# Performance work log

Hardware: AMD Instinct MI355X
Metric: run time of the kernel (lower is better)

## Reference

```python
import jax, jax.numpy as jnp
import numpy as np
import math

B, L, D = 8, 2048, 768
ORDER, EMB = 128, 5
FFT = 2 * L
MIN_DECAY = math.log(0.01) / 1.5   # slow_decay_pct = 1.5
MAX_DECAY = math.log(0.01) / 0.3   # fast_decay_pct = 0.3
SHIFT = 0.0


def _pos_emb(seq_len, emb_dim):
    # pos_emb_init from the source: [t, Re(z), Im(z)] with bands = (emb_dim-1)//2
    bands = (emb_dim - 1) // 2
    t = jnp.linspace(0.0, 1.0, seq_len)[None, :, None]
    t_res = jnp.linspace(0.0, seq_len - 1, seq_len)[None, :, None]
    w = 2.0 * jnp.pi * t_res / seq_len
    f = jnp.linspace(1e-4, bands - 1, bands)[None, None]
    zc = jnp.exp(-1j * f * w)
    return jnp.concatenate([t, zc.real, zc.imag], axis=-1).astype(jnp.float32)  # (1, L, EMB)


def setup_inputs() -> dict:
    key = jax.random.key(0)
    ks = jax.random.split(key, 16)
    s = 0.02
    return {
        "u": jax.random.normal(ks[0], (B, L, D), jnp.float32),
        "in_W": jax.random.normal(ks[1], (D, 3 * D), jnp.float32) * s,
        "in_b": jnp.zeros((3 * D,), jnp.float32),
        "out_W": jax.random.normal(ks[2], (D, D), jnp.float32) * s,
        "out_b": jnp.zeros((D,), jnp.float32),
        "x1_s": jax.random.normal(ks[3], (D, 4), jnp.float32) * 0.25,
        "x2_s": jax.random.normal(ks[4], (D, 4), jnp.float32) * 0.25,
        "v_s": jax.random.normal(ks[5], (D, 4), jnp.float32) * 0.25,
        "x1_sb": jax.random.normal(ks[6], (D,), jnp.float32) * 0.1,
        "x2_sb": jax.random.normal(ks[7], (D,), jnp.float32) * 0.1,
        "v_sb": jax.random.normal(ks[8], (D,), jnp.float32) * 0.1,
        "D_bias": jax.random.normal(ks[9], (D,), jnp.float32),
        "z": _pos_emb(L, EMB),
        "sin_freq": 10.0 * jnp.ones((1, ORDER), jnp.float32),   # hyena_w = 10
        "eo_mat": jax.random.normal(ks[10], (1, EMB, ORDER), jnp.float32) * 0.3,
        "eo_bias": jnp.zeros((1, ORDER), jnp.float32),
        "oo1_mat": jax.random.normal(ks[11], (1, ORDER, ORDER), jnp.float32) * 0.08,
        "oo1_bias": jnp.zeros((1, ORDER), jnp.float32),
        "oo2_mat": jax.random.normal(ks[12], (1, ORDER, ORDER), jnp.float32) * 0.08,
        "oo2_bias": jnp.zeros((1, ORDER), jnp.float32),
        "oh_mat": jax.random.normal(ks[13], (1, ORDER, D), jnp.float32) * 0.08,
    }


def _depthwise4(x, w, b):
    # torch Conv1d(groups=3D, kernel=4, padding=3) truncated to [:L] == causal conv, left pad 3
    out = jax.lax.conv_general_dilated(
        x, w[:, None, :], window_strides=(1,), padding=[(3, 0)],
        dimension_numbers=("NCH", "OIH", "NCH"), feature_group_count=x.shape[1])
    return out + b[None, :, None]


def _hyena_filter(z, sin_freq, eo_mat, eo_bias, oo1_mat, oo1_bias, oo2_mat, oo2_bias, oh_mat):
    # then exponential decay modulation (exp_mod_in_place_fwd), channels=1, reverse=0.
    f = sin_freq[:, None, :]                                       # (1, 1, ORDER)
    h = jnp.sin(f * (jnp.einsum("cle,ceo->clo", z, eo_mat) + eo_bias[:, None, :]))
    h = jnp.sin(f * (jnp.einsum("clo,cop->clp", h, oo1_mat) + oo1_bias[:, None, :]))
    h = jnp.sin(f * (jnp.einsum("clo,cop->clp", h, oo2_mat) + oo2_bias[:, None, :]))
    k = jnp.einsum("clo,coh->clh", h, oh_mat)                      # (1, L, D)
    t = jnp.linspace(0.0, 1.0, k.shape[1])
    deltas = jnp.abs(jnp.linspace(MIN_DECAY, MAX_DECAY, k.shape[2]))
    k = k * (jnp.exp(-t[None, :, None] * deltas[None, None, :]) + SHIFT)
    return k[0].T                                                  # (D, L)


def _forward(u, in_W, in_b, out_W, out_b, x1_s, x2_s, v_s, x1_sb, x2_sb, v_sb,
             D_bias, z, sin_freq, eo_mat, eo_bias, oo1_mat, oo1_bias,
             oo2_mat, oo2_bias, oh_mat):
    seqlen = u.shape[1]
    k = _hyena_filter(z, sin_freq, eo_mat, eo_bias, oo1_mat, oo1_bias, oo2_mat, oo2_bias, oh_mat)
    x1x2v = u @ in_W + in_b                                        # (B, L, 3D)
    x1, x2, v = jnp.split(x1x2v, 3, axis=-1)
    x1 = jnp.transpose(x1, (0, 2, 1))                              # (B, D, L)
    x2 = jnp.transpose(x2, (0, 2, 1))
    v = jnp.transpose(v, (0, 2, 1))
    x1 = _depthwise4(x1, x1_s, x1_sb)
    x2 = _depthwise4(x2, x2_s, x2_sb)
    v = _depthwise4(v, v_s, v_sb)
    v = v * x1                                                     # first gate
    k_f = jnp.fft.rfft(k.astype(jnp.float32), n=FFT)               # (D, FFT//2+1)
    v_f = jnp.fft.rfft(v.astype(jnp.float32), n=FFT)               # (B, D, FFT//2+1)
    y = jnp.fft.irfft(v_f * k_f[None], n=FFT)[..., :seqlen]        # long FFT conv
    y = y + v * D_bias[None, :, None]                              # skip term
    y = y * x2                                                     # second gate
    y = jnp.transpose(y, (0, 2, 1))                                # (B, L, D)
    return y @ out_W + out_b


def reference(u, in_W, in_b, out_W, out_b, x1_s, x2_s, v_s, x1_sb, x2_sb, v_sb,
              D_bias, z, sin_freq, eo_mat, eo_bias, oo1_mat, oo1_bias,
              oo2_mat, oo2_bias, oh_mat):
    return _forward(u, in_W, in_b, out_W, out_b, x1_s, x2_s, v_s, x1_sb, x2_sb, v_sb,
                    D_bias, z, sin_freq, eo_mat, eo_bias, oo1_mat, oo1_bias,
                    oo2_mat, oo2_bias, oh_mat)
```

## Files before the change

### kernel.cpp

```cpp
#include <hip/hip_runtime.h>


typedef __bf16 bf16x8 __attribute__((ext_vector_type(8)));
typedef float  f32x4  __attribute__((ext_vector_type(4)));

#define AS1 __attribute__((address_space(1)))
#define AS3 __attribute__((address_space(3)))
#define GLD16(gp, lp) __builtin_amdgcn_global_load_lds((AS1 void*)(void*)(gp), (AS3 void*)(void*)(lp), 16, 0, 0)

#define PIPE_VM_BARRIER(N)  __asm__ __volatile__("s_waitcnt vmcnt(" #N ")\n\ts_barrier" ::: "memory")
#define PIPE_LGKM_BARRIER   __asm__ __volatile__("s_waitcnt lgkmcnt(0)\n\ts_barrier" ::: "memory")

__device__ __forceinline__ unsigned short f2b(float f) {
    unsigned u = __builtin_bit_cast(unsigned, f);
    unsigned r = (u + 0x7fffu + ((u >> 16) & 1u)) >> 16;
    return (unsigned short)r;
}
__device__ __forceinline__ float b2f(unsigned short h) {
    unsigned u = ((unsigned)h) << 16;
    return __builtin_bit_cast(float, u);
}
__device__ __forceinline__ float b2f_lo(unsigned u) {
    return __builtin_bit_cast(float, u << 16);
}
__device__ __forceinline__ float b2f_hi(unsigned u) {
    return __builtin_bit_cast(float, u & 0xffff0000u);
}

__device__ __forceinline__ float2 cmul(float2 a, float2 b) {
    return make_float2(a.x * b.x - a.y * b.y, a.x * b.y + a.y * b.x);
}
__device__ __forceinline__ float2 cadd(float2 a, float2 b) { return make_float2(a.x + b.x, a.y + b.y); }
__device__ __forceinline__ float2 csub(float2 a, float2 b) { return make_float2(a.x - b.x, a.y - b.y); }

#define BFLY(i,j)   { float2 ta=x[i], tb=x[j]; x[i]=cadd(ta,tb); x[j]=csub(ta,tb); }
#define BFLYW(i,j,w){ float2 ta=x[i], tb=x[j]; x[i]=cadd(ta,tb); x[j]=cmul(csub(ta,tb),(w)); }
#define BFLYI(i,j)  { float2 ta=x[i], tb=x[j]; x[i]=cadd(ta,tb); float2 tt=csub(ta,tb); x[j]=make_float2(-dd*tt.y, dd*tt.x); }
#define CSWAP(i,j)  { float2 tt=x[i]; x[i]=x[j]; x[j]=tt; }

template<int DIR, bool UZ>
__device__ __forceinline__ void dft16(float2* x) {
    const float dd = (float)DIR;
    const float C1 = 0.92387953251128674f, S1 = 0.38268343236508977f, R2 = 0.70710678118654752f;
    const float2 W1 = make_float2( C1, dd*S1);
    const float2 W2 = make_float2( R2, dd*R2);
    const float2 W3 = make_float2( S1, dd*C1);
    const float2 W5 = make_float2(-S1, dd*C1);
    const float2 W6 = make_float2(-R2, dd*R2);
    const float2 W7 = make_float2(-C1, dd*S1);
    if (UZ) {
        x[8]  = x[0];
        x[9]  = cmul(x[1], W1);
        x[10] = cmul(x[2], W2);
        x[11] = cmul(x[3], W3);
        x[12] = make_float2(-dd*x[4].y, dd*x[4].x);
        x[13] = cmul(x[5], W5);
        x[14] = cmul(x[6], W6);
        x[15] = cmul(x[7], W7);
    } else {
        BFLY(0,8); BFLYW(1,9,W1); BFLYW(2,10,W2); BFLYW(3,11,W3);
        BFLYI(4,12); BFLYW(5,13,W5); BFLYW(6,14,W6); BFLYW(7,15,W7);
    }
    BFLY(0,4);  BFLYW(1,5,W2);  BFLYI(2,6);   BFLYW(3,7,W6);
    BFLY(8,12); BFLYW(9,13,W2); BFLYI(10,14); BFLYW(11,15,W6);
    BFLY(0,2);  BFLYI(1,3);  BFLY(4,6);   BFLYI(5,7);
    BFLY(8,10); BFLYI(9,11); BFLY(12,14); BFLYI(13,15);
    BFLY(0,1); BFLY(2,3); BFLY(4,5); BFLY(6,7);
    BFLY(8,9); BFLY(10,11); BFLY(12,13); BFLY(14,15);
    CSWAP(1,8); CSWAP(2,4); CSWAP(3,12); CSWAP(5,10); CSWAP(7,14); CSWAP(11,13);
}

__device__ __forceinline__ void twiddle_mul(float2* x, float ang) {
    float s, c; __sincosf(ang, &s, &c);
    float2 w[16];
    w[1] = make_float2(c, s);
    w[2] = cmul(w[1], w[1]);
    w[3] = cmul(w[2], w[1]);  w[4] = cmul(w[2], w[2]);
    w[5] = cmul(w[4], w[1]);  w[6] = cmul(w[4], w[2]);
    w[7] = cmul(w[4], w[3]);  w[8] = cmul(w[4], w[4]);
    w[9]  = cmul(w[8], w[1]); w[10] = cmul(w[8], w[2]);
    w[11] = cmul(w[8], w[3]); w[12] = cmul(w[8], w[4]);
    w[13] = cmul(w[8], w[5]); w[14] = cmul(w[8], w[6]);
    w[15] = cmul(w[8], w[7]);
    #pragma unroll
    for (int k = 1; k < 16; ++k) x[k] = cmul(x[k], w[k]);
}

#define TWO_PI 6.283185307179586f
__device__ __forceinline__ void fft4096_fwd(float2* x, float2* lds, int t) {
    dft16<-1, true>(x);
    twiddle_mul(x, -(float)t * (TWO_PI / 4096.0f));
    #pragma unroll
    for (int k1 = 0; k1 < 16; ++k1) lds[k1 * 272 + t] = x[k1];
    __syncthreads();
    const int hi = t >> 4, lo = t & 15;
    #pragma unroll
    for (int t1 = 0; t1 < 16; ++t1) x[t1] = lds[hi * 272 + t1 * 16 + lo];
    dft16<-1, false>(x);
    twiddle_mul(x, -(float)lo * (TWO_PI / 256.0f));
    __syncthreads();
    #pragma unroll
    for (int k2 = 0; k2 < 16; ++k2) lds[t * 17 + k2] = x[k2];
    __syncthreads();
    #pragma unroll
    for (int t0 = 0; t0 < 16; ++t0) x[t0] = lds[(hi * 16 + t0) * 17 + lo];
    dft16<-1, false>(x);
}

__device__ __forceinline__ void fft4096_inv(float2* x, float2* lds, int t) {
    const int hi = t >> 4, lo = t & 15;
    dft16<1, false>(x);
    __syncthreads();
    #pragma unroll
    for (int t0 = 0; t0 < 16; ++t0) lds[(hi * 16 + t0) * 17 + lo] = x[t0];
    __syncthreads();
    #pragma unroll
    for (int k2 = 0; k2 < 16; ++k2) x[k2] = lds[t * 17 + k2];
    twiddle_mul(x, (float)lo * (TWO_PI / 256.0f));
    dft16<1, false>(x);
    __syncthreads();
    #pragma unroll
    for (int t1 = 0; t1 < 16; ++t1) lds[hi * 272 + t1 * 16 + lo] = x[t1];
    __syncthreads();
    #pragma unroll
    for (int k1 = 0; k1 < 16; ++k1) x[k1] = lds[k1 * 272 + t];
    twiddle_mul(x, (float)t * (TWO_PI / 4096.0f));
    dft16<1, false>(x);
}

__global__ __launch_bounds__(256) void filter_k_kernel(
    const float* __restrict__ z, const float* __restrict__ sf,
    const float* __restrict__ eo, const float* __restrict__ eo_b,
    const float* __restrict__ oo1, const float* __restrict__ oo1_b,
    const float* __restrict__ oo2, const float* __restrict__ oo2_b,
    const float* __restrict__ oh, float* __restrict__ kfil)
{
    __shared__ float h3buf[8][128];
    __shared__ float htmp[2][128];
    const int t = threadIdx.x;
    const int l0 = blockIdx.x * 8;
    const int half = t >> 7;
    const int o = t & 127;
    const float sfo = sf[o];
    for (int p = 0; p < 4; ++p) {
        const int li = p * 2 + half;
        const int l = l0 + li;
        float a = eo_b[o];
        #pragma unroll
        for (int e = 0; e < 5; ++e) a += z[l * 5 + e] * eo[e * 128 + o];
        htmp[half][o] = sinf(sfo * a);
        __syncthreads();
        float a2 = oo1_b[o];
        for (int q = 0; q < 128; ++q) a2 += htmp[half][q] * oo1[q * 128 + o];
        const float h2 = sinf(sfo * a2);
        __syncthreads();
        htmp[half][o] = h2;
        __syncthreads();
        float a3 = oo2_b[o];
        for (int q = 0; q < 128; ++q) a3 += htmp[half][q] * oo2[q * 128 + o];
        h3buf[li][o] = sinf(sfo * a3);
        __syncthreads();
    }
    const float MIND = -3.070113457325394f;
    const float MAXD = -15.350567286626972f;
    for (int c = 0; c < 3; ++c) {
        const int h = t + c * 256;
        float acc[8];
        #pragma unroll
        for (int li = 0; li < 8; ++li) acc[li] = 0.f;
        for (int q = 0; q < 128; ++q) {
            const float w = oh[q * 768 + h];
            #pragma unroll
            for (int li = 0; li < 8; ++li) acc[li] += h3buf[li][q] * w;
        }
        const float delta = fabsf(MIND + (MAXD - MIND) * (float)h * (1.0f / 767.0f));
        #pragma unroll
        for (int li = 0; li < 8; ++li) {
            const int l = l0 + li;
            const float tt = (float)l * (1.0f / 2047.0f);
            kfil[h * 2048 + l] = acc[li] * expf(-tt * delta);
        }
    }
}

__global__ __launch_bounds__(256, 4) void filter_fft_kernel(
    const float* __restrict__ kfil, float2* __restrict__ Kf)
{
    __shared__ float2 lds[4352];
    const int d = blockIdx.x, t = threadIdx.x;
    float2 x[16];
    #pragma unroll
    for (int r = 0; r < 8; ++r) x[r] = make_float2(kfil[d * 2048 + r * 256 + t], 0.f);
    fft4096_fwd(x, lds, t);
    #pragma unroll
    for (int k3 = 0; k3 < 16; ++k3) Kf[d * 4096 + k3 * 256 + t] = x[k3];
}

__global__ __launch_bounds__(256) void convert_u_kernel(
    const float* __restrict__ u, unsigned short* __restrict__ ub)
{
    const int g = blockIdx.x * 256 + threadIdx.x;
    const float4 v = ((const float4*)u)[g];
    uint2 o;
    o.x = (unsigned)f2b(v.x) | ((unsigned)f2b(v.y) << 16);
    o.y = (unsigned)f2b(v.z) | ((unsigned)f2b(v.w) << 16);
    ((uint2*)ub)[g] = o;
}

__global__ __launch_bounds__(256) void transpose_W_kernel(
    const float* __restrict__ W, unsigned short* __restrict__ Wt, int K, int N)
{
    __shared__ float tile[32][33];
    const int n0 = blockIdx.x * 32, k0 = blockIdx.y * 32;
    const int tx = threadIdx.x & 31, ty = threadIdx.x >> 5;
    #pragma unroll
    for (int r = 0; r < 4; ++r) {
        const int kk = ty + r * 8;
        tile[kk][tx] = W[(k0 + kk) * N + n0 + tx];
    }
    __syncthreads();
    #pragma unroll
    for (int r = 0; r < 4; ++r) {
        const int nn = ty + r * 8;
        Wt[(n0 + nn) * K + k0 + tx] = f2b(tile[tx][nn]);
    }
}

__global__ __launch_bounds__(256) void transpose_Y_kernel(
    const unsigned short* __restrict__ Y, unsigned short* __restrict__ Yt)
{
    __shared__ unsigned short tile[32][34];
    const int bx = blockIdx.x;
    const int l0 = (bx & 63) * 32;
    const int tmp = bx >> 6;
    const int d0 = (tmp % 24) * 32;
    const int b  = tmp / 24;
    const int tx = threadIdx.x & 31, ty = threadIdx.x >> 5;
    #pragma unroll
    for (int r = 0; r < 4; ++r) {
        const int dd = ty + r * 8;
        tile[dd][tx] = Y[(b * 768 + d0 + dd) * 2048 + l0 + tx];
    }
    __syncthreads();
    #pragma unroll
    for (int r = 0; r < 4; ++r) {
        const int ll = ty + r * 8;
        Yt[(b * 2048 + l0 + ll) * 768 + d0 + tx] = tile[tx][ll];
    }
}

__global__ __launch_bounds__(256, 3) void gemm_kernel(
    const unsigned short* __restrict__ A,
    const unsigned short* __restrict__ Bm,
    const float* __restrict__ bias,
    unsigned short* __restrict__ outb,
    float* __restrict__ outf,
    int mode)
{
    __shared__ __align__(16) unsigned short As[3 * 4096];
    __shared__ __align__(16) unsigned short Bs[3 * 4096];
    const int t = threadIdx.x;
    const int wv = t >> 6, lane = t & 63;
    const int row0 = (mode == 0 ? blockIdx.y : blockIdx.x) * 128;
    const int col0 = (mode == 0 ? blockIdx.x : blockIdx.y) * 128;
    const int wr = wv >> 1, wc = wv & 1;

    f32x4 acc[4][4] = {};

    const int r0 = t >> 2;
    const int r1 = r0 + 64;
    const int c0 = (t & 3) ^ (((r0 >> 1) ^ (r0 >> 3)) & 3);
    const int c1 = (t & 3) ^ (((r1 >> 1) ^ (r1 >> 3)) & 3);
    const unsigned short* gA0 = A + (row0 + r0) * 768 + c0 * 8;
    const unsigned short* gA1 = A + (row0 + r1) * 768 + c1 * 8;
    const unsigned short* gB0 = Bm + (col0 + r0) * 768 + c0 * 8;
    const unsigned short* gB1 = Bm + (col0 + r1) * 768 + c1 * 8;

    const int frow = lane & 15, kc = lane >> 4;
    int offA[4], offB[4];
    #pragma unroll
    for (int i = 0; i < 4; ++i) {
        const int ra = wr * 64 + i * 16 + frow;
        const int rb = wc * 64 + i * 16 + frow;
        offA[i] = ra * 32 + ((kc ^ (((ra >> 1) ^ (ra >> 3)) & 3)) << 3);
        offB[i] = rb * 32 + ((kc ^ (((rb >> 1) ^ (rb >> 3)) & 3)) << 3);
    }

    GLD16(gA0, (char*)As + wv * 1024);
    GLD16(gA1, (char*)As + 4096 + wv * 1024);
    GLD16(gB0, (char*)Bs + wv * 1024);
    GLD16(gB1, (char*)Bs + 4096 + wv * 1024);
    gA0 += 32; gA1 += 32; gB0 += 32; gB1 += 32;
    GLD16(gA0, (char*)As + 8192 + wv * 1024);
    GLD16(gA1, (char*)As + 8192 + 4096 + wv * 1024);
    GLD16(gB0, (char*)Bs + 8192 + wv * 1024);
    GLD16(gB1, (char*)Bs + 8192 + 4096 + wv * 1024);
    gA0 += 32; gA1 += 32; gB0 += 32; gB1 += 32;

#define GEMM_FRAG_MFMA(CUR)                                                   \
        const unsigned short* Ast = As + (CUR) * 4096;                        \
        const unsigned short* Bst = Bs + (CUR) * 4096;                        \
        bf16x8 af[4], bfr[4];                                                 \
        _Pragma("unroll") for (int i = 0; i < 4; ++i) {                       \
            af[i]  = *(const bf16x8*)(Ast + offA[i]);                         \
            bfr[i] = *(const bf16x8*)(Bst + offB[i]);                         \
        }                                                                     \
        _Pragma("unroll") for (int i = 0; i < 4; ++i)                         \
            _Pragma("unroll") for (int j = 0; j < 4; ++j)                     \
                acc[i][j] = __builtin_amdgcn_mfma_f32_16x16x32_bf16(          \
                    af[i], bfr[j], acc[i][j], 0, 0, 0);

#define GEMM_BODY(CUR, PF)                                                    \
    {                                                                         \
        GLD16(gA0, (char*)As + (PF) * 8192 + wv * 1024);                      \
        GLD16(gA1, (char*)As + (PF) * 8192 + 4096 + wv * 1024);               \
        GLD16(gB0, (char*)Bs + (PF) * 8192 + wv * 1024);                      \
        GLD16(gB1, (char*)Bs + (PF) * 8192 + 4096 + wv * 1024);               \
        gA0 += 32; gA1 += 32; gB0 += 32; gB1 += 32;                           \
        PIPE_VM_BARRIER(8);     \
        GEMM_FRAG_MFMA(CUR)                                                   \
        PIPE_LGKM_BARRIER;     \
    }

#define GEMM_TAIL(CUR, N)                                                     \
    {                                                                         \
        PIPE_VM_BARRIER(N);                                                   \
        GEMM_FRAG_MFMA(CUR)                                                   \
    }

    for (int kq = 0; kq < 7; ++kq) {
        GEMM_BODY(0, 2)
        GEMM_BODY(1, 0)
        GEMM_BODY(2, 1)
    }
    GEMM_BODY(0, 2)
    GEMM_TAIL(1, 4)
    GEMM_TAIL(2, 0)
#undef GEMM_BODY
#undef GEMM_TAIL
#undef GEMM_FRAG_MFMA

    if (mode == 0) {
        const int part = row0 / 768;
        const int bb = col0 / 2048;
        unsigned short* Xp = outb + (part * 8 + bb) * 768 * 2048;
        const int dbase = row0 - part * 768 + wr * 64 + (lane >> 4) * 4;
        const int lbase = col0 - bb * 2048 + wc * 64 + frow;
        #pragma unroll
        for (int i = 0; i < 4; ++i) {
            #pragma unroll
            for (int rr = 0; rr < 4; ++rr) {
                const int dd = dbase + i * 16 + rr;
                const float bn = bias[row0 + wr * 64 + (lane >> 4) * 4 + i * 16 + rr];
                #pragma unroll
                for (int j = 0; j < 4; ++j) {
                    const int ll = lbase + j * 16;
                    Xp[dd * 2048 + ll] = f2b(acc[i][j][rr] + bn);
                }
            }
        }
    } else {
        #pragma unroll
        for (int i = 0; i < 4; ++i) {
            #pragma unroll
            for (int rr = 0; rr < 4; ++rr) {
                const int m = row0 + wr * 64 + (lane >> 4) * 4 + i * 16 + rr;
                #pragma unroll
                for (int j = 0; j < 4; ++j) {
                    const int n = col0 + wc * 64 + j * 16 + frow;
                    outf[m * 768 + n] = acc[i][j][rr] + bias[n];
                }
            }
        }
    }
}

__device__ __forceinline__ void conv6(const unsigned short* __restrict__ p,
                                      const float* w, float bias, int t, float* out8)
{
    const uint4 m = *(const uint4*)(p + 8 * t);
    uint2 q = make_uint2(0u, 0u);
    if (t) q = *(const uint2*)(p + 8 * t - 4);
    float s[12];
    s[0] = b2f_lo(q.x); s[1] = b2f_hi(q.x); s[2] = b2f_lo(q.y); s[3] = b2f_hi(q.y);
    s[4] = b2f_lo(m.x); s[5] = b2f_hi(m.x); s[6] = b2f_lo(m.y); s[7] = b2f_hi(m.y);
    s[8] = b2f_lo(m.z); s[9] = b2f_hi(m.z); s[10] = b2f_lo(m.w); s[11] = b2f_hi(m.w);
    #pragma unroll
    for (int i = 0; i < 8; ++i)
        out8[i] = bias + w[0] * s[i + 1] + w[1] * s[i + 2] + w[2] * s[i + 3] + w[3] * s[i + 4];
}

__global__ __launch_bounds__(256, 4) void fft_conv_kernel(
    const unsigned short* __restrict__ X, const float2* __restrict__ Kf,
    const float* __restrict__ x1_s, const float* __restrict__ x2_s, const float* __restrict__ v_s,
    const float* __restrict__ x1_sb, const float* __restrict__ x2_sb, const float* __restrict__ v_sb,
    const float* __restrict__ D_bias, unsigned short* __restrict__ Y)
{
    __shared__ __align__(16) float2 lds[4352];
    unsigned* ldsu = (unsigned*)lds;
    const int d = blockIdx.x, jp = blockIdx.y, t = threadIdx.x;
    const int b0 = jp * 2, b1 = b0 + 1;

    float w1[4], w2[4], wv[4];
    #pragma unroll
    for (int j = 0; j < 4; ++j) { w1[j] = x1_s[d * 4 + j]; w2[j] = x2_s[d * 4 + j]; wv[j] = v_s[d * 4 + j]; }
    const float bc1 = x1_sb[d], bc2 = x2_sb[d], bcv = v_sb[d], Db = D_bias[d];

    const unsigned short* px1a = X + ((size_t)(0 * 8 + b0) * 768 + d) * 2048;
    const unsigned short* px2a = X + ((size_t)(1 * 8 + b0) * 768 + d) * 2048;
    const unsigned short* pva  = X + ((size_t)(2 * 8 + b0) * 768 + d) * 2048;
    const unsigned short* px1b = X + ((size_t)(0 * 8 + b1) * 768 + d) * 2048;
    const unsigned short* px2b = X + ((size_t)(1 * 8 + b1) * 768 + d) * 2048;
    const unsigned short* pvb  = X + ((size_t)(2 * 8 + b1) * 768 + d) * 2048;

    {
        float x1a[8], x2a[8], vva[8];
        conv6(px1a, w1, bc1, t, x1a);
        conv6(px2a, w2, bc2, t, x2a);
        conv6(pva,  wv, bcv, t, vva);
        float x1b[8], x2b[8], vvb[8];
        conv6(px1b, w1, bc1, t, x1b);
        conv6(px2b, w2, bc2, t, x2b);
        conv6(pvb,  wv, bcv, t, vvb);
        unsigned vh_pk[8], c2_pk[8];
        #pragma unroll
        for (int i = 0; i < 8; ++i) {
            vh_pk[i] = (unsigned)f2b(vva[i] * x1a[i]) | ((unsigned)f2b(vvb[i] * x1b[i]) << 16);
            c2_pk[i] = (unsigned)f2b(x2a[i]) | ((unsigned)f2b(x2b[i]) << 16);
        }
        *(uint4*)(ldsu + 8 * t)        = make_uint4(vh_pk[0], vh_pk[1], vh_pk[2], vh_pk[3]);
        *(uint4*)(ldsu + 8 * t + 4)    = make_uint4(vh_pk[4], vh_pk[5], vh_pk[6], vh_pk[7]);
        *(uint4*)(ldsu + 2048 + 8 * t)     = make_uint4(c2_pk[0], c2_pk[1], c2_pk[2], c2_pk[3]);
        *(uint4*)(ldsu + 2048 + 8 * t + 4) = make_uint4(c2_pk[4], c2_pk[5], c2_pk[6], c2_pk[7]);
    }
    __syncthreads();

    unsigned vhp[8], c2p[8];
    float2 x[16];
    #pragma unroll
    for (int r = 0; r < 8; ++r) {
        const unsigned u = ldsu[r * 256 + t];
        vhp[r] = u;
        x[r] = make_float2(b2f_lo(u), b2f_hi(u));
    }
    #pragma unroll
    for (int r = 0; r < 8; ++r) c2p[r] = ldsu[2048 + r * 256 + t];

    const float2* kf = Kf + (size_t)d * 4096;
    float2 kfr[16];
    #pragma unroll
    for (int k3 = 0; k3 < 16; ++k3) kfr[k3] = kf[k3 * 256 + t];

    __syncthreads();

    fft4096_fwd(x, lds, t);
    #pragma unroll
    for (int k3 = 0; k3 < 16; ++k3) x[k3] = cmul(x[k3], kfr[k3]);
    fft4096_inv(x, lds, t);

    const float invN = 1.0f / 4096.0f;
    unsigned short* ya = Y + ((size_t)b0 * 768 + d) * 2048;
    unsigned short* yb = Y + ((size_t)b1 * 768 + d) * 2048;
    #pragma unroll
    for (int n1 = 0; n1 < 8; ++n1) {
        const int l = n1 * 256 + t;
        const float va = b2f_lo(vhp[n1]);
        const float vb = b2f_hi(vhp[n1]);
        const float ca = b2f_lo(c2p[n1]);
        const float cb = b2f_hi(c2p[n1]);
        ya[l] = f2b((x[n1].x * invN + va * Db) * ca);
        yb[l] = f2b((x[n1].y * invN + vb * Db) * cb);
    }
}

extern "C" void kernel_launch(void* const* d_in, const int* in_sizes, int n_in,
                              void* d_out, int out_size, void* d_ws, size_t ws_size,
                              hipStream_t stream)
{
    (void)in_sizes; (void)n_in; (void)out_size; (void)ws_size;
    const float* u      = (const float*)d_in[0];
    const float* in_W   = (const float*)d_in[1];
    const float* in_b   = (const float*)d_in[2];
    const float* out_W  = (const float*)d_in[3];
    const float* out_b  = (const float*)d_in[4];
    const float* x1_s   = (const float*)d_in[5];
    const float* x2_s   = (const float*)d_in[6];
    const float* v_s    = (const float*)d_in[7];
    const float* x1_sb  = (const float*)d_in[8];
    const float* x2_sb  = (const float*)d_in[9];
    const float* v_sb   = (const float*)d_in[10];
    const float* D_bias = (const float*)d_in[11];
    const float* z      = (const float*)d_in[12];
    const float* sf     = (const float*)d_in[13];
    const float* eo     = (const float*)d_in[14];
    const float* eo_b   = (const float*)d_in[15];
    const float* oo1    = (const float*)d_in[16];
    const float* oo1_b  = (const float*)d_in[17];
    const float* oo2    = (const float*)d_in[18];
    const float* oo2_b  = (const float*)d_in[19];
    const float* oh     = (const float*)d_in[20];
    float* out = (float*)d_out;

    char* ws = (char*)d_ws;
    unsigned short* Xbf  = (unsigned short*)(ws + 0);
    unsigned short* Ybf  = (unsigned short*)(ws + 75497472);
    unsigned short* ubYt = (unsigned short*)(ws + 100663296);
    unsigned short* Wt   = (unsigned short*)(ws + 125829120);
    unsigned short* W2t  = (unsigned short*)(ws + 129368064);
    float*          kfil = (float*)(ws + 130547712);
    float2*         Kf   = (float2*)(ws + 136839168);

    filter_k_kernel<<<256, 256, 0, stream>>>(z, sf, eo, eo_b, oo1, oo1_b, oo2, oo2_b, oh, kfil);
    filter_fft_kernel<<<768, 256, 0, stream>>>(kfil, Kf);
    convert_u_kernel<<<12288, 256, 0, stream>>>(u, ubYt);
    transpose_W_kernel<<<dim3(72, 24), 256, 0, stream>>>(in_W, Wt, 768, 2304);
    transpose_W_kernel<<<dim3(24, 24), 256, 0, stream>>>(out_W, W2t, 768, 768);
    gemm_kernel<<<dim3(128, 18), 256, 0, stream>>>(Wt, ubYt, in_b, Xbf, nullptr, 0);
    fft_conv_kernel<<<dim3(768, 4), 256, 0, stream>>>(Xbf, Kf, x1_s, x2_s, v_s, x1_sb, x2_sb, v_sb, D_bias, Ybf);
    transpose_Y_kernel<<<12288, 256, 0, stream>>>(Ybf, ubYt);
    gemm_kernel<<<dim3(128, 6), 256, 0, stream>>>(ubYt, W2t, out_b, nullptr, out, 1);
}
```

Baseline: 402.1 us.

## Replace GEMM with 256x256-tile, 512-thread double-buffered MFMA kernel

Rewrites both projection GEMMs to use 256x256 output tiles with 8 waves and 64-wide K stages in 128KB of dynamic LDS. Loads for the next K stage are interleaved at a fine grain with quarter-tile MFMA groups, and MFMA sections run at raised wave priority. The larger tile cuts global and LDS traffic per FLOP. In exchange there are fewer blocks (576 and 192), which may underfill the GPU's CUs and cause tail effects, and register pressure goes up.

Measured after the change: 395.7 us. About the same (-1.6%).

```diff
diff --git a/kernel.cpp b/kernel.cpp
--- a/kernel.cpp
+++ b/kernel.cpp
@@ -8,8 +8,8 @@
 #define AS3 __attribute__((address_space(3)))
 #define GLD16(gp, lp) __builtin_amdgcn_global_load_lds((AS1 void*)(void*)(gp), (AS3 void*)(void*)(lp), 16, 0, 0)
 
-#define PIPE_VM_BARRIER(N)  __asm__ __volatile__("s_waitcnt vmcnt(" #N ")\n\ts_barrier" ::: "memory")
-#define PIPE_LGKM_BARRIER   __asm__ __volatile__("s_waitcnt lgkmcnt(0)\n\ts_barrier" ::: "memory")
+#define LGKM_BAR       __asm__ __volatile__("s_waitcnt lgkmcnt(0)\n\ts_barrier" ::: "memory")
+#define VM_LGKM_BAR(N) __asm__ __volatile__("s_waitcnt vmcnt(" #N ") lgkmcnt(0)\n\ts_barrier" ::: "memory")
 
 __device__ __forceinline__ unsigned short f2b(float f) {
     unsigned u = __builtin_bit_cast(unsigned, f);
@@ -249,7 +249,7 @@
     }
 }
 
-__global__ __launch_bounds__(256, 3) void gemm_kernel(
+__global__ __launch_bounds__(512, 2) void gemm256_kernel(
     const unsigned short* __restrict__ A,
     const unsigned short* __restrict__ Bm,
     const float* __restrict__ bias,
@@ -257,118 +257,149 @@
     float* __restrict__ outf,
     int mode)
 {
-    __shared__ __align__(16) unsigned short As[3 * 4096];
-    __shared__ __align__(16) unsigned short Bs[3 * 4096];
+    extern __shared__ __align__(16) unsigned short lds[];
+    unsigned short* As = lds;
+    unsigned short* Bs = lds + 32768;
     const int t = threadIdx.x;
     const int wv = t >> 6, lane = t & 63;
-    const int row0 = (mode == 0 ? blockIdx.y : blockIdx.x) * 128;
-    const int col0 = (mode == 0 ? blockIdx.x : blockIdx.y) * 128;
-    const int wr = wv >> 1, wc = wv & 1;
-
-    f32x4 acc[4][4] = {};
-
-    const int r0 = t >> 2;
-    const int r1 = r0 + 64;
-    const int c0 = (t & 3) ^ (((r0 >> 1) ^ (r0 >> 3)) & 3);
-    const int c1 = (t & 3) ^ (((r1 >> 1) ^ (r1 >> 3)) & 3);
-    const unsigned short* gA0 = A + (row0 + r0) * 768 + c0 * 8;
-    const unsigned short* gA1 = A + (row0 + r1) * 768 + c1 * 8;
-    const unsigned short* gB0 = Bm + (col0 + r0) * 768 + c0 * 8;
-    const unsigned short* gB1 = Bm + (col0 + r1) * 768 + c1 * 8;
-
+    const int row0 = (mode == 0 ? blockIdx.y : blockIdx.x) * 256;
+    const int col0 = (mode == 0 ? blockIdx.x : blockIdx.y) * 256;
+    const int wr = wv >> 2, wc = wv & 3;
     const int frow = lane & 15, kc = lane >> 4;
-    int offA[4], offB[4];
-    #pragma unroll
-    for (int i = 0; i < 4; ++i) {
-        const int ra = wr * 64 + i * 16 + frow;
-        const int rb = wc * 64 + i * 16 + frow;
-        offA[i] = ra * 32 + ((kc ^ (((ra >> 1) ^ (ra >> 3)) & 3)) << 3);
-        offB[i] = rb * 32 + ((kc ^ (((rb >> 1) ^ (rb >> 3)) & 3)) << 3);
-    }
-
-    GLD16(gA0, (char*)As + wv * 1024);
-    GLD16(gA1, (char*)As + 4096 + wv * 1024);
-    GLD16(gB0, (char*)Bs + wv * 1024);
-    GLD16(gB1, (char*)Bs + 4096 + wv * 1024);
-    gA0 += 32; gA1 += 32; gB0 += 32; gB1 += 32;
-    GLD16(gA0, (char*)As + 8192 + wv * 1024);
-    GLD16(gA1, (char*)As + 8192 + 4096 + wv * 1024);
-    GLD16(gB0, (char*)Bs + 8192 + wv * 1024);
-    GLD16(gB1, (char*)Bs + 8192 + 4096 + wv * 1024);
-    gA0 += 32; gA1 += 32; gB0 += 32; gB1 += 32;
-
-#define GEMM_FRAG_MFMA(CUR)                                                   \
-        const unsigned short* Ast = As + (CUR) * 4096;                        \
-        const unsigned short* Bst = Bs + (CUR) * 4096;                        \
-        bf16x8 af[4], bfr[4];                                                 \
-        _Pragma("unroll") for (int i = 0; i < 4; ++i) {                       \
-            af[i]  = *(const bf16x8*)(Ast + offA[i]);                         \
-            bfr[i] = *(const bf16x8*)(Bst + offB[i]);                         \
-        }                                                                     \
-        _Pragma("unroll") for (int i = 0; i < 4; ++i)                         \
-            _Pragma("unroll") for (int j = 0; j < 4; ++j)                     \
-                acc[i][j] = __builtin_amdgcn_mfma_f32_16x16x32_bf16(          \
-                    af[i], bfr[j], acc[i][j], 0, 0, 0);
-
-#define GEMM_BODY(CUR, PF)                                                    \
-    {                                                                         \
-        GLD16(gA0, (char*)As + (PF) * 8192 + wv * 1024);                      \
-        GLD16(gA1, (char*)As + (PF) * 8192 + 4096 + wv * 1024);               \
-        GLD16(gB0, (char*)Bs + (PF) * 8192 + wv * 1024);                      \
-        GLD16(gB1, (char*)Bs + (PF) * 8192 + 4096 + wv * 1024);               \
-        gA0 += 32; gA1 += 32; gB0 += 32; gB1 += 32;                           \
-        PIPE_VM_BARRIER(8);     \
-        GEMM_FRAG_MFMA(CUR)                                                   \
-        PIPE_LGKM_BARRIER;     \
-    }
-
-#define GEMM_TAIL(CUR, N)                                                     \
-    {                                                                         \
-        PIPE_VM_BARRIER(N);                                                   \
-        GEMM_FRAG_MFMA(CUR)                                                   \
-    }
-
-    for (int kq = 0; kq < 7; ++kq) {
-        GEMM_BODY(0, 2)
-        GEMM_BODY(1, 0)
-        GEMM_BODY(2, 1)
-    }
-    GEMM_BODY(0, 2)
-    GEMM_TAIL(1, 4)
-    GEMM_TAIL(2, 0)
-#undef GEMM_BODY
-#undef GEMM_TAIL
-#undef GEMM_FRAG_MFMA
+
+    f32x4 acc[8][4] = {};
+
+    const int srow = t >> 3;
+    const int cdat = (t & 7) ^ (srow & 7);
+    const unsigned short* gA = A  + (row0 + srow) * 768 + cdat * 8;
+    const unsigned short* gB = Bm + (col0 + srow) * 768 + cdat * 8;
+
+#define STG_A(buf, q, koff) GLD16(gA + (q) * 49152 + (koff), (char*)As + (buf) * 32768 + (q) * 8192 + wv * 1024)
+#define STG_B(buf, q, koff) GLD16(gB + (q) * 49152 + (koff), (char*)Bs + (buf) * 32768 + (q) * 8192 + wv * 1024)
+
+    const int sx = frow & 7;
+    const int aRowBase = (wr * 128 + frow) * 64;
+    const int bRowBase = (wc * 64 + frow) * 64;
+    const int sl0 = ((0 + kc) ^ sx) * 8;
+    const int sl1 = ((4 + kc) ^ sx) * 8;
+
+    bf16x8 aF[4][2], bN0[2][2], bN1[2][2];
+
+#define READ_A(buf, mh)                                                         \
+    _Pragma("unroll") for (int m = 0; m < 4; ++m) {                             \
+        aF[m][0] = *(const bf16x8*)(As + (buf) * 16384 + aRowBase + ((mh) * 4 + m) * 1024 + sl0); \
+        aF[m][1] = *(const bf16x8*)(As + (buf) * 16384 + aRowBase + ((mh) * 4 + m) * 1024 + sl1); \
+    }
+#define READ_B(buf, nh, arr)                                                    \
+    _Pragma("unroll") for (int n = 0; n < 2; ++n) {                             \
+        arr[n][0] = *(const bf16x8*)(Bs + (buf) * 16384 + bRowBase + ((nh) * 2 + n) * 1024 + sl0); \
+        arr[n][1] = *(const bf16x8*)(Bs + (buf) * 16384 + bRowBase + ((nh) * 2 + n) * 1024 + sl1); \
+    }
+#define MFMA_Q(mh, nh, arr)                                                     \
+    __builtin_amdgcn_s_setprio(1);                                              \
+    _Pragma("unroll") for (int m = 0; m < 4; ++m)                               \
+    _Pragma("unroll") for (int n = 0; n < 2; ++n)                               \
+    _Pragma("unroll") for (int ks = 0; ks < 2; ++ks)                            \
+        acc[(mh) * 4 + m][(nh) * 2 + n] = __builtin_amdgcn_mfma_f32_16x16x32_bf16( \
+            aF[m][ks], arr[n][ks], acc[(mh) * 4 + m][(nh) * 2 + n], 0, 0, 0);   \
+    __builtin_amdgcn_s_setprio(0);
+
+    STG_A(0, 0, 0); STG_A(0, 1, 0); STG_A(0, 2, 0); STG_A(0, 3, 0);
+    STG_B(0, 0, 0); STG_B(0, 1, 0); STG_B(0, 2, 0); STG_B(0, 3, 0);
+    STG_A(1, 0, 64); STG_A(1, 2, 64);
+    STG_B(1, 0, 64); STG_B(1, 1, 64); STG_B(1, 2, 64); STG_B(1, 3, 64);
+    VM_LGKM_BAR(6);
+
+    for (int i = 0; i < 5; ++i) {
+        const int k1 = (2 * i + 1) * 64, k2 = (2 * i + 2) * 64, k3 = (2 * i + 3) * 64;
+        READ_A(0, 0); READ_B(0, 0, bN0);
+        STG_A(1, 1, k1); STG_A(1, 3, k1);
+        MFMA_Q(0, 0, bN0);
+        LGKM_BAR;
+        READ_B(0, 1, bN1);
+        STG_A(0, 0, k2); STG_A(0, 2, k2);
+        MFMA_Q(0, 1, bN1);
+        LGKM_BAR;
+        READ_A(0, 1);
+        STG_B(0, 0, k2); STG_B(0, 1, k2);
+        MFMA_Q(1, 1, bN1);
+        LGKM_BAR;
+        STG_B(0, 2, k2); STG_B(0, 3, k2);
+        MFMA_Q(1, 0, bN0);
+        VM_LGKM_BAR(6);
+        READ_A(1, 0); READ_B(1, 0, bN0);
+        STG_A(0, 1, k2); STG_A(0, 3, k2);
+        MFMA_Q(0, 0, bN0);
+        LGKM_BAR;
+        READ_B(1, 1, bN1);
+        STG_A(1, 0, k3); STG_A(1, 2, k3);
+        MFMA_Q(0, 1, bN1);
+        LGKM_BAR;
+        READ_A(1, 1);
+        STG_B(1, 0, k3); STG_B(1, 1, k3);
+        MFMA_Q(1, 1, bN1);
+        LGKM_BAR;
+        STG_B(1, 2, k3); STG_B(1, 3, k3);
+        MFMA_Q(1, 0, bN0);
+        VM_LGKM_BAR(6);
+    }
+
+    {
+        READ_A(0, 0); READ_B(0, 0, bN0);
+        STG_A(1, 1, 704); STG_A(1, 3, 704);
+        MFMA_Q(0, 0, bN0);
+        LGKM_BAR;
+        READ_B(0, 1, bN1);
+        MFMA_Q(0, 1, bN1);
+        LGKM_BAR;
+        READ_A(0, 1);
+        MFMA_Q(1, 1, bN1);
+        LGKM_BAR;
+        MFMA_Q(1, 0, bN0);
+        VM_LGKM_BAR(2);
+        READ_A(1, 0); READ_B(1, 0, bN0);
+        MFMA_Q(0, 0, bN0);
+        LGKM_BAR;
+        READ_B(1, 1, bN1);
+        MFMA_Q(0, 1, bN1);
+        VM_LGKM_BAR(0);
+        READ_A(1, 1);
+        MFMA_Q(1, 1, bN1);
+        MFMA_Q(1, 0, bN0);
+    }
+#undef READ_A
+#undef READ_B
+#undef MFMA_Q
+#undef STG_A
+#undef STG_B
 
     if (mode == 0) {
         const int part = row0 / 768;
         const int bb = col0 / 2048;
-        unsigned short* Xp = outb + (part * 8 + bb) * 768 * 2048;
-        const int dbase = row0 - part * 768 + wr * 64 + (lane >> 4) * 4;
-        const int lbase = col0 - bb * 2048 + wc * 64 + frow;
+        unsigned short* Xp = outb + (size_t)(part * 8 + bb) * 768 * 2048;
+        const int drow0 = row0 - part * 768 + wr * 128 + (lane >> 4) * 4;
+        const int lcol0 = col0 - bb * 2048 + wc * 64 + frow;
         #pragma unroll
-        for (int i = 0; i < 4; ++i) {
+        for (int m = 0; m < 8; ++m) {
             #pragma unroll
             for (int rr = 0; rr < 4; ++rr) {
-                const int dd = dbase + i * 16 + rr;
-                const float bn = bias[row0 + wr * 64 + (lane >> 4) * 4 + i * 16 + rr];
+                const int dd = drow0 + m * 16 + rr;
+                const float bn = bias[row0 + wr * 128 + (lane >> 4) * 4 + m * 16 + rr];
                 #pragma unroll
-                for (int j = 0; j < 4; ++j) {
-                    const int ll = lbase + j * 16;
-                    Xp[dd * 2048 + ll] = f2b(acc[i][j][rr] + bn);
-                }
+                for (int n = 0; n < 4; ++n)
+                    Xp[dd * 2048 + lcol0 + n * 16] = f2b(acc[m][n][rr] + bn);
             }
         }
     } else {
         #pragma unroll
-        for (int i = 0; i < 4; ++i) {
+        for (int m = 0; m < 8; ++m) {
             #pragma unroll
             for (int rr = 0; rr < 4; ++rr) {
-                const int m = row0 + wr * 64 + (lane >> 4) * 4 + i * 16 + rr;
+                const int mm = row0 + wr * 128 + (lane >> 4) * 4 + m * 16 + rr;
                 #pragma unroll
-                for (int j = 0; j < 4; ++j) {
-                    const int n = col0 + wc * 64 + j * 16 + frow;
-                    outf[m * 768 + n] = acc[i][j][rr] + bias[n];
+                for (int n = 0; n < 4; ++n) {
+                    const int nn = col0 + wc * 64 + n * 16 + frow;
+                    outf[(size_t)mm * 768 + nn] = acc[m][n][rr] + bias[nn];
                 }
             }
         }
@@ -510,13 +541,20 @@
     float*          kfil = (float*)(ws + 130547712);
     float2*         Kf   = (float2*)(ws + 136839168);
 
+    static int attr_set = 0;
+    if (!attr_set) {
+        (void)hipFuncSetAttribute(reinterpret_cast<const void*>(gemm256_kernel),
+                                  hipFuncAttributeMaxDynamicSharedMemorySize, 131072);
+        attr_set = 1;
+    }
+
     filter_k_kernel<<<256, 256, 0, stream>>>(z, sf, eo, eo_b, oo1, oo1_b, oo2, oo2_b, oh, kfil);
     filter_fft_kernel<<<768, 256, 0, stream>>>(kfil, Kf);
     convert_u_kernel<<<12288, 256, 0, stream>>>(u, ubYt);
     transpose_W_kernel<<<dim3(72, 24), 256, 0, stream>>>(in_W, Wt, 768, 2304);
     transpose_W_kernel<<<dim3(24, 24), 256, 0, stream>>>(out_W, W2t, 768, 768);
-    gemm_kernel<<<dim3(128, 18), 256, 0, stream>>>(Wt, ubYt, in_b, Xbf, nullptr, 0);
+    gemm256_kernel<<<dim3(64, 9), 512, 131072, stream>>>(Wt, ubYt, in_b, Xbf, nullptr, 0);
     fft_conv_kernel<<<dim3(768, 4), 256, 0, stream>>>(Xbf, Kf, x1_s, x2_s, v_s, x1_sb, x2_sb, v_sb, D_bias, Ybf);
     transpose_Y_kernel<<<12288, 256, 0, stream>>>(Ybf, ubYt);
-    gemm_kernel<<<dim3(128, 6), 256, 0, stream>>>(ubYt, W2t, out_b, nullptr, out, 1);
-}
+    gemm256_kernel<<<dim3(64, 3), 512, 131072, stream>>>(ubYt, W2t, out_b, nullptr, out, 1);
+}
```
